# Optimization experiments

Measured on AMD Instinct MI355X. Metric: run time of the kernel, lower is better.

Reference implementation:

```python
import jax, jax.numpy as jnp
import numpy as np

PI = 3.14159  # constant as written in the source
V = 10        # node count hard-coded by the module


def setup_inputs() -> dict:
    key = jax.random.key(0)
    ks = jax.random.split(key, 10)
    B, T, F = 128, 200, 256
    end_output = jax.random.normal(ks[0], (B, T, V, F), dtype=jnp.float32)
    S = jax.random.uniform(ks[1], (B, T, V, V), dtype=jnp.float32)  # values in [0,1)
    mul = jax.random.normal(ks[2], (V, V), dtype=jnp.float32) * 0.05
    bias = jax.random.normal(ks[3], (V, V), dtype=jnp.float32) * 0.05
    means = jax.random.normal(ks[4], (1, V), dtype=jnp.float32) * 0.05
    stds = 0.5 + jax.random.uniform(ks[5], (1, V), dtype=jnp.float32)  # keep away from 0
    emb_in = jax.random.normal(ks[6], (F, F), dtype=jnp.float32) * 0.05
    emb_out = jax.random.normal(ks[7], (F, F), dtype=jnp.float32) * 0.05
    emb3 = jax.random.normal(ks[8], (V, V), dtype=jnp.float32) * 0.05
    emb4 = jax.random.normal(ks[9], (V, V), dtype=jnp.float32) * 0.05
    return {"end_output": end_output, "S": S, "mul": mul, "bias": bias,
            "means": means, "stds": stds, "emb_in": emb_in, "emb_out": emb_out,
            "emb3": emb3, "emb4": emb4}


def reference(end_output, S, mul, bias, means, stds, emb_in, emb_out, emb3, emb4):
    # end_output: (B,T,V,F), S: (B,T,V,V)
    S = jnp.minimum(S, jnp.swapaxes(S, -1, -2))  # symmetrize

    # GaussianLayer: K.dot(S, mul) + bias, gaussian pdf, sigmoid, then tanh
    x = jnp.einsum('btij,jk->btik', S, mul) + bias
    a = (2.0 * PI) ** 0.5
    tmp = jnp.exp(-0.5 * ((x - means) / stds) ** 2) / (a * stds)
    edge_feature = jnp.tanh(jax.nn.sigmoid(tmp))  # (B,T,V,V)

    # Degree (centrality) embedding: D = K.sum(A, axis=1) -> sum over rows
    D = jnp.sum(S, axis=-2)  # (B,T,V)
    Di = jax.lax.stop_gradient(D).astype(jnp.int32)
    outputs = end_output + emb_in[Di] + emb_out[Di]  # (B,T,V,F)

    # Floyd-Warshall APSP, vectorized over (B,T); accumulate update-indicator * edge_feature
    dist = S
    sp = jnp.zeros_like(S)
    for k in range(V):
        temp = dist[..., :, k:k + 1] + dist[..., k:k + 1, :]  # dist[i,k] + dist[k,j]
        new = jnp.minimum(dist, temp)
        upd = (new != dist).astype(dist.dtype)  # 1 where relaxed
        sp = sp + upd * edge_feature
        dist = new

    Spatial_i = jax.lax.stop_gradient(dist).astype(jnp.int32)  # (B,T,V,V) in [0,V)
    Edge_i = jax.lax.stop_gradient(sp).astype(jnp.int32)       # (B,T,V,V) in [0,V)
    Spatial_Encoding = jnp.sum(emb3[Spatial_i], axis=-2)  # (B,T,V,10)
    Edge_Encoding = jnp.sum(emb4[Edge_i], axis=-2)         # (B,T,V,10)
    atten_bias = Edge_Encoding + Spatial_Encoding
    return outputs, atten_bias
```

## Files before the change

kernel.cpp:

```cpp
#include <hip/hip_runtime.h>
#include <math.h>

constexpr int NV  = 10;
constexpr int NF  = 256;
constexpr int NC  = NV * NV;
constexpr int GPB = 4;

typedef float v4f __attribute__((ext_vector_type(4)));

__global__ __launch_bounds__(256) void graph_emb_fused(
    const float* __restrict__ end_output,
    const float* __restrict__ S,
    const float* __restrict__ mul,
    const float* __restrict__ bias,
    const float* __restrict__ means,
    const float* __restrict__ stds,
    const float* __restrict__ emb_in,
    const float* __restrict__ emb_out,
    const float* __restrict__ emb3,
    const float* __restrict__ emb4,
    float* __restrict__ out_main,
    float* __restrict__ out_atten,
    int BT)
{
    __shared__ __attribute__((aligned(16))) float s_embsum[NV * NF];
    __shared__ float s_mul[NC], s_bias[NC], s_emb3[NC], s_emb4[NC];
    __shared__ float s_means[NV], s_stds[NV];
    __shared__ float s_dist[GPB][NC];
    __shared__ int   s_si[GPB][NC];
    __shared__ int   s_ei[GPB][NC];
    __shared__ int   s_Di[GPB][NV];

    const int tid   = threadIdx.x;
    const int wave  = tid >> 6;
    const int lane  = tid & 63;
    const int gbase = blockIdx.x * GPB;
    const int g     = gbase + wave;

    for (int idx = tid; idx < NV * NF; idx += 256)
        s_embsum[idx] = emb_in[idx] + emb_out[idx];
    if (tid < NC) {
        s_mul[tid]  = mul[tid];
        s_bias[tid] = bias[tid];
        s_emb3[tid] = emb3[tid];
        s_emb4[tid] = emb4[tid];
    }
    if (tid >= 128 && tid < 128 + NV) {
        s_means[tid - 128] = means[tid - 128];
        s_stds[tid - 128]  = stds[tid - 128];
    }

    const int c0 = lane;
    const int c1 = 64 + lane;
    const bool has1 = (lane < 36);
    const int i0 = c0 / NV, j0 = c0 % NV;
    const int i1 = c1 / NV, j1 = c1 % NV;

    if (g < BT) {
        const int g0 = g * NC;
        s_dist[wave][c0] = fminf(S[g0 + c0], S[g0 + j0 * NV + i0]);
        if (has1)
            s_dist[wave][c1] = fminf(S[g0 + c1], S[g0 + j1 * NV + i1]);

        if (lane < NV) {
            float d = 0.f;
            #pragma unroll
            for (int i = 0; i < NV; ++i) d += s_dist[wave][i * NV + lane];
            int di = (int)d;
            s_Di[wave][lane] = min(max(di, 0), NV - 1);
        }
    }

    __syncthreads();

    {
        const size_t slab = (size_t)gbase * (NV * NF);
        const v4f* end4 = reinterpret_cast<const v4f*>(end_output + slab);
        v4f*       out4 = reinterpret_cast<v4f*>(out_main + slab);
        const v4f* es4  = reinterpret_cast<const v4f*>(s_embsum);
        const int* sdi  = &s_Di[0][0];

        if (gbase + GPB <= BT) {
            #pragma unroll
            for (int it = 0; it < NV; ++it) {
                const int chunk = it * GPB + wave;
                const int u     = (chunk << 6) + lane;
                v4f e = __builtin_nontemporal_load(end4 + u);
                v4f s = es4[sdi[chunk] * (NF / 4) + lane];
                e += s;
                __builtin_nontemporal_store(e, out4 + u);
            }
        } else {
            const int ng    = BT - gbase;
            const int items = ng * (NV * NF / 4);
            for (int u = tid; u < items; u += 256) {
                int gg = u / 640, rem = u - gg * 640;
                int row = rem >> 6, f4 = rem & 63;
                v4f e = __builtin_nontemporal_load(end4 + u);
                v4f s = es4[sdi[gg * NV + row] * (NF / 4) + f4];
                e += s;
                __builtin_nontemporal_store(e, out4 + u);
            }
        }
    }

    if (g < BT) {
        const int g0 = g * NC;

        const float A = sqrtf(2.0f * 3.14159f);
        float ef0 = 0.f, ef1 = 0.f, sp0 = 0.f, sp1 = 0.f;
        {
            float acc = 0.f;
            #pragma unroll
            for (int j = 0; j < NV; ++j)
                acc += s_dist[wave][i0 * NV + j] * s_mul[j * NV + j0];
            float x = acc + s_bias[c0];
            float z = (x - s_means[j0]) / s_stds[j0];
            float tmp = expf(-0.5f * z * z) / (A * s_stds[j0]);
            float sg = 1.0f / (1.0f + expf(-tmp));
            ef0 = tanhf(sg);
        }
        if (has1) {
            float acc = 0.f;
            #pragma unroll
            for (int j = 0; j < NV; ++j)
                acc += s_dist[wave][i1 * NV + j] * s_mul[j * NV + j1];
            float x = acc + s_bias[c1];
            float z = (x - s_means[j1]) / s_stds[j1];
            float tmp = expf(-0.5f * z * z) / (A * s_stds[j1]);
            float sg = 1.0f / (1.0f + expf(-tmp));
            ef1 = tanhf(sg);
        }

        #pragma unroll
        for (int k = 0; k < NV; ++k) {
            float t0 = s_dist[wave][i0 * NV + k] + s_dist[wave][k * NV + j0];
            if (t0 < s_dist[wave][c0]) { s_dist[wave][c0] = t0; sp0 += ef0; }
            if (has1) {
                float t1 = s_dist[wave][i1 * NV + k] + s_dist[wave][k * NV + j1];
                if (t1 < s_dist[wave][c1]) { s_dist[wave][c1] = t1; sp1 += ef1; }
            }
        }

        {
            int si = (int)s_dist[wave][c0];
            int ei = (int)sp0;
            s_si[wave][c0] = min(max(si, 0), NV - 1);
            s_ei[wave][c0] = min(max(ei, 0), NV - 1);
        }
        if (has1) {
            int si = (int)s_dist[wave][c1];
            int ei = (int)sp1;
            s_si[wave][c1] = min(max(si, 0), NV - 1);
            s_ei[wave][c1] = min(max(ei, 0), NV - 1);
        }

        {
            float acc3 = 0.f, acc4 = 0.f;
            #pragma unroll
            for (int j = 0; j < NV; ++j) {
                acc3 += s_emb3[s_si[wave][i0 * NV + j] * NV + j0];
                acc4 += s_emb4[s_ei[wave][i0 * NV + j] * NV + j0];
            }
            __builtin_nontemporal_store(acc4 + acc3, out_atten + g0 + c0);
        }
        if (has1) {
            float acc3 = 0.f, acc4 = 0.f;
            #pragma unroll
            for (int j = 0; j < NV; ++j) {
                acc3 += s_emb3[s_si[wave][i1 * NV + j] * NV + j1];
                acc4 += s_emb4[s_ei[wave][i1 * NV + j] * NV + j1];
            }
            __builtin_nontemporal_store(acc4 + acc3, out_atten + g0 + c1);
        }
    }
}

extern "C" void kernel_launch(void* const* d_in, const int* in_sizes, int n_in,
                              void* d_out, int out_size, void* d_ws, size_t ws_size,
                              hipStream_t stream) {
    const float* end_output = (const float*)d_in[0];
    const float* S          = (const float*)d_in[1];
    const float* mul        = (const float*)d_in[2];
    const float* bias       = (const float*)d_in[3];
    const float* means      = (const float*)d_in[4];
    const float* stds       = (const float*)d_in[5];
    const float* emb_in     = (const float*)d_in[6];
    const float* emb_out    = (const float*)d_in[7];
    const float* emb3       = (const float*)d_in[8];
    const float* emb4       = (const float*)d_in[9];

    float* out_main  = (float*)d_out;
    float* out_atten = out_main + (size_t)in_sizes[0];

    const int BT = in_sizes[1] / (NV * NV);
    const int nblocks = (BT + GPB - 1) / GPB;

    graph_emb_fused<<<nblocks, 256, 0, stream>>>(
        end_output, S, mul, bias, means, stds,
        emb_in, emb_out, emb3, emb4, out_main, out_atten, BT);
}
```

Before: 458.5 us.

## Split fused kernel into graph-math and streaming-add kernels via workspace

Splits the single fused kernel into two launches. The first computes the symmetrized graph math (degree indices, Floyd-Warshall, attention bias) and writes degree indices and the summed embedding table to workspace. The second is a pure streaming kernel that adds the selected embedding rows to end_output. The aim is to stop the latency-bound per-graph math from stalling the bandwidth-bound streaming, at the cost of an extra launch and a small workspace round trip. The old fused kernel is kept as a fallback when the workspace is too small.

```diff
diff --git a/kernel.cpp b/kernel.cpp
--- a/kernel.cpp
+++ b/kernel.cpp
@@ -7,6 +7,194 @@
 constexpr int GPB = 4;
 
 typedef float v4f __attribute__((ext_vector_type(4)));
+
+
+__global__ __launch_bounds__(256) void graph_math(
+    const float* __restrict__ S,
+    const float* __restrict__ mul,
+    const float* __restrict__ bias,
+    const float* __restrict__ means,
+    const float* __restrict__ stds,
+    const float* __restrict__ emb_in,
+    const float* __restrict__ emb_out,
+    const float* __restrict__ emb3,
+    const float* __restrict__ emb4,
+    float* __restrict__ out_atten,
+    int*   __restrict__ Di_ws,
+    float* __restrict__ es_ws,
+    int BT)
+{
+    __shared__ float s_mul[NC], s_bias[NC], s_emb3[NC], s_emb4[NC];
+    __shared__ float s_means[NV], s_stds[NV];
+    __shared__ float s_dist[GPB][NC];
+    __shared__ int   s_si[GPB][NC];
+    __shared__ int   s_ei[GPB][NC];
+
+    const int tid   = threadIdx.x;
+    const int wave  = tid >> 6;
+    const int lane  = tid & 63;
+    const int gbase = blockIdx.x * GPB;
+    const int g     = gbase + wave;
+
+    if (blockIdx.x == 0) {
+        for (int idx = tid; idx < NV * NF; idx += 256)
+            es_ws[idx] = emb_in[idx] + emb_out[idx];
+    }
+
+    if (tid < NC) {
+        s_mul[tid]  = mul[tid];
+        s_bias[tid] = bias[tid];
+        s_emb3[tid] = emb3[tid];
+        s_emb4[tid] = emb4[tid];
+    }
+    if (tid >= 128 && tid < 128 + NV) {
+        s_means[tid - 128] = means[tid - 128];
+        s_stds[tid - 128]  = stds[tid - 128];
+    }
+    __syncthreads();
+
+    if (g >= BT) return;
+
+    const int c0 = lane;
+    const int c1 = 64 + lane;
+    const bool has1 = (lane < 36);
+    const int i0 = c0 / NV, j0 = c0 % NV;
+    const int i1 = c1 / NV, j1 = c1 % NV;
+    const int g0 = g * NC;
+
+    s_dist[wave][c0] = fminf(S[g0 + c0], S[g0 + j0 * NV + i0]);
+    if (has1)
+        s_dist[wave][c1] = fminf(S[g0 + c1], S[g0 + j1 * NV + i1]);
+
+    if (lane < NV) {
+        float d = 0.f;
+        #pragma unroll
+        for (int i = 0; i < NV; ++i) d += s_dist[wave][i * NV + lane];
+        int di = (int)d;
+        Di_ws[g * NV + lane] = min(max(di, 0), NV - 1);
+    }
+
+    const float A = sqrtf(2.0f * 3.14159f);
+    float ef0 = 0.f, ef1 = 0.f, sp0 = 0.f, sp1 = 0.f;
+    {
+        float acc = 0.f;
+        #pragma unroll
+        for (int j = 0; j < NV; ++j)
+            acc += s_dist[wave][i0 * NV + j] * s_mul[j * NV + j0];
+        float x = acc + s_bias[c0];
+        float z = (x - s_means[j0]) / s_stds[j0];
+        float tmp = expf(-0.5f * z * z) / (A * s_stds[j0]);
+        float sg = 1.0f / (1.0f + expf(-tmp));
+        ef0 = tanhf(sg);
+    }
+    if (has1) {
+        float acc = 0.f;
+        #pragma unroll
+        for (int j = 0; j < NV; ++j)
+            acc += s_dist[wave][i1 * NV + j] * s_mul[j * NV + j1];
+        float x = acc + s_bias[c1];
+        float z = (x - s_means[j1]) / s_stds[j1];
+        float tmp = expf(-0.5f * z * z) / (A * s_stds[j1]);
+        float sg = 1.0f / (1.0f + expf(-tmp));
+        ef1 = tanhf(sg);
+    }
+
+    #pragma unroll
+    for (int k = 0; k < NV; ++k) {
+        float t0 = s_dist[wave][i0 * NV + k] + s_dist[wave][k * NV + j0];
+        if (t0 < s_dist[wave][c0]) { s_dist[wave][c0] = t0; sp0 += ef0; }
+        if (has1) {
+            float t1 = s_dist[wave][i1 * NV + k] + s_dist[wave][k * NV + j1];
+            if (t1 < s_dist[wave][c1]) { s_dist[wave][c1] = t1; sp1 += ef1; }
+        }
+    }
+
+    {
+        int si = (int)s_dist[wave][c0];
+        int ei = (int)sp0;
+        s_si[wave][c0] = min(max(si, 0), NV - 1);
+        s_ei[wave][c0] = min(max(ei, 0), NV - 1);
+    }
+    if (has1) {
+        int si = (int)s_dist[wave][c1];
+        int ei = (int)sp1;
+        s_si[wave][c1] = min(max(si, 0), NV - 1);
+        s_ei[wave][c1] = min(max(ei, 0), NV - 1);
+    }
+
+    {
+        float acc3 = 0.f, acc4 = 0.f;
+        #pragma unroll
+        for (int j = 0; j < NV; ++j) {
+            acc3 += s_emb3[s_si[wave][i0 * NV + j] * NV + j0];
+            acc4 += s_emb4[s_ei[wave][i0 * NV + j] * NV + j0];
+        }
+        __builtin_nontemporal_store(acc4 + acc3, out_atten + g0 + c0);
+    }
+    if (has1) {
+        float acc3 = 0.f, acc4 = 0.f;
+        #pragma unroll
+        for (int j = 0; j < NV; ++j) {
+            acc3 += s_emb3[s_si[wave][i1 * NV + j] * NV + j1];
+            acc4 += s_emb4[s_ei[wave][i1 * NV + j] * NV + j1];
+        }
+        __builtin_nontemporal_store(acc4 + acc3, out_atten + g0 + c1);
+    }
+}
+
+__global__ __launch_bounds__(256) void stream_add(
+    const float* __restrict__ end_output,
+    const int*   __restrict__ Di_ws,
+    const float* __restrict__ es_ws,
+    float* __restrict__ out_main,
+    int BT)
+{
+    __shared__ __attribute__((aligned(16))) float s_es[NV * NF];
+    __shared__ int s_di[GPB * NV];
+
+    const int tid   = threadIdx.x;
+    const int wave  = tid >> 6;
+    const int lane  = tid & 63;
+    const int gbase = blockIdx.x * GPB;
+
+    {
+        v4f* d4 = reinterpret_cast<v4f*>(s_es);
+        const v4f* s4 = reinterpret_cast<const v4f*>(es_ws);
+        for (int idx = tid; idx < NV * NF / 4; idx += 256)
+            d4[idx] = s4[idx];
+        const int ng = min(GPB, BT - gbase);
+        if (tid < ng * NV) s_di[tid] = Di_ws[gbase * NV + tid];
+    }
+    __syncthreads();
+
+    const size_t slab = (size_t)gbase * (NV * NF);
+    const v4f* end4 = reinterpret_cast<const v4f*>(end_output + slab);
+    v4f*       out4 = reinterpret_cast<v4f*>(out_main + slab);
+    const v4f* es4  = reinterpret_cast<const v4f*>(s_es);
+
+    if (gbase + GPB <= BT) {
+        #pragma unroll
+        for (int it = 0; it < NV; ++it) {
+            const int chunk = it * GPB + wave;
+            const int u     = (chunk << 6) + lane;
+            v4f e = __builtin_nontemporal_load(end4 + u);
+            v4f s = es4[s_di[chunk] * (NF / 4) + lane];
+            e += s;
+            __builtin_nontemporal_store(e, out4 + u);
+        }
+    } else {
+        const int ng    = BT - gbase;
+        const int items = ng * (NV * NF / 4);
+        for (int u = tid; u < items; u += 256) {
+            int gg = u / 640, rem = u - gg * 640;
+            int row = rem >> 6, f4 = rem & 63;
+            v4f e = __builtin_nontemporal_load(end4 + u);
+            v4f s = es4[s_di[gg * NV + row] * (NF / 4) + f4];
+            e += s;
+            __builtin_nontemporal_store(e, out4 + u);
+        }
+    }
+}
 
 __global__ __launch_bounds__(256) void graph_emb_fused(
     const float* __restrict__ end_output,
@@ -61,7 +249,6 @@
         s_dist[wave][c0] = fminf(S[g0 + c0], S[g0 + j0 * NV + i0]);
         if (has1)
             s_dist[wave][c1] = fminf(S[g0 + c1], S[g0 + j1 * NV + i1]);
-
         if (lane < NV) {
             float d = 0.f;
             #pragma unroll
@@ -70,7 +257,6 @@
             s_Di[wave][lane] = min(max(di, 0), NV - 1);
         }
     }
-
     __syncthreads();
 
     {
@@ -106,7 +292,6 @@
 
     if (g < BT) {
         const int g0 = g * NC;
-
         const float A = sqrtf(2.0f * 3.14159f);
         float ef0 = 0.f, ef1 = 0.f, sp0 = 0.f, sp1 = 0.f;
         {
@@ -131,7 +316,6 @@
             float sg = 1.0f / (1.0f + expf(-tmp));
             ef1 = tanhf(sg);
         }
-
         #pragma unroll
         for (int k = 0; k < NV; ++k) {
             float t0 = s_dist[wave][i0 * NV + k] + s_dist[wave][k * NV + j0];
@@ -141,7 +325,6 @@
                 if (t1 < s_dist[wave][c1]) { s_dist[wave][c1] = t1; sp1 += ef1; }
             }
         }
-
         {
             int si = (int)s_dist[wave][c0];
             int ei = (int)sp0;
@@ -154,7 +337,6 @@
             s_si[wave][c1] = min(max(si, 0), NV - 1);
             s_ei[wave][c1] = min(max(ei, 0), NV - 1);
         }
-
         {
             float acc3 = 0.f, acc4 = 0.f;
             #pragma unroll
@@ -196,7 +378,20 @@
     const int BT = in_sizes[1] / (NV * NV);
     const int nblocks = (BT + GPB - 1) / GPB;
 
-    graph_emb_fused<<<nblocks, 256, 0, stream>>>(
-        end_output, S, mul, bias, means, stds,
-        emb_in, emb_out, emb3, emb4, out_main, out_atten, BT);
+    const size_t di_bytes = ((size_t)BT * NV * sizeof(int) + 15) & ~(size_t)15;
+    const size_t need     = di_bytes + (size_t)NV * NF * sizeof(float);
+
+    if (d_ws != nullptr && ws_size >= need) {
+        int*   Di_ws = (int*)d_ws;
+        float* es_ws = (float*)((char*)d_ws + di_bytes);
+        graph_math<<<nblocks, 256, 0, stream>>>(
+            S, mul, bias, means, stds, emb_in, emb_out, emb3, emb4,
+            out_atten, Di_ws, es_ws, BT);
+        stream_add<<<nblocks, 256, 0, stream>>>(
+            end_output, Di_ws, es_ws, out_main, BT);
+    } else {
+        graph_emb_fused<<<nblocks, 256, 0, stream>>>(
+            end_output, S, mul, bias, means, stds,
+            emb_in, emb_out, emb3, emb4, out_main, out_atten, BT);
+    }
 }
```

Result: no change. 467.3 us (+1.9%).
